# Kernel tuning notes

Hardware: AMD Instinct MI355X
Metric: run time of the kernel (lower is better)

Reference implementation:

```python
import jax, jax.numpy as jnp
import numpy as np

N_BINS = 64
SIGMA_SCALE = 0.5
_LAB_RANGES = {'L': (0.0, 100.0), 'a': (-128.0, 127.0), 'b': (-128.0, 127.0)}


def _channel_params(vmin, vmax, n_bins=N_BINS, sigma_scale=SIGMA_SCALE):
    delta = (vmax - vmin) / n_bins
    centers = jnp.linspace(vmin + delta / 2, vmax - delta / 2, n_bins, dtype=jnp.float32)
    sigma = jnp.float32(delta * sigma_scale)
    return centers, sigma


def rgb_to_lab(rgb):
    # rgb: (B, 3, H, W) in [0, 1] sRGB
    thr = 0.04045
    lin = jnp.where(rgb > thr, jnp.power((rgb + 0.055) / 1.055, 2.4), rgb / 12.92)
    r, g, b = lin[:, 0], lin[:, 1], lin[:, 2]
    # sRGB -> XYZ (D65)
    x = 0.412453 * r + 0.357580 * g + 0.180423 * b
    y = 0.212671 * r + 0.715160 * g + 0.072169 * b
    z = 0.019334 * r + 0.119193 * g + 0.950227 * b
    xn, zn = 0.950456, 1.088754  # D65 white (Y normalized to 1)
    x = x / xn
    z = z / zn
    eps = 0.008856
    def f(t):
        return jnp.where(t > eps, jnp.cbrt(t), 7.787 * t + 16.0 / 116.0)
    fx, fy, fz = f(x), f(y), f(z)
    L = 116.0 * fy - 16.0
    a = 500.0 * (fx - fy)
    bb = 200.0 * (fy - fz)
    return jnp.stack([L, a, bb], axis=1)  # (B, 3, H, W)


def setup_inputs() -> dict:
    key = jax.random.key(0)
    img = jax.random.uniform(key, (16, 3, 512, 512), dtype=jnp.float32)
    return {"img": img}


def reference(img) -> jnp.ndarray:
    B = img.shape[0]
    img_lab = rgb_to_lab(img)  # (B, 3, H, W)
    parts = []
    for c_idx, name in enumerate(['L', 'a', 'b']):
        centers, sigma = _channel_params(*_LAB_RANGES[name])
        pixels = img_lab[:, c_idx].reshape(B, -1)  # (B, HW)
        diff = pixels[:, :, None] - centers[None, None, :]  # (B, HW, n_bins)
        weights = jnp.exp(-(diff ** 2) / (2.0 * sigma ** 2))
        hist_unnorm = weights.sum(axis=1)  # (B, n_bins)
        hist = hist_unnorm / (hist_unnorm.sum(axis=-1, keepdims=True) + 1e-8)
        parts.append(hist)
    return jnp.concatenate(parts, axis=1)  # (B, 192)
```

## Files before the change

kernel.cpp:

```cpp
#include <hip/hip_runtime.h>
#include <cmath>

#define HW (512*512)
#define NSUB 2048
#define THREADS1 1024
#define BLKS_PER_IMG 32

__global__ __launch_bounds__(THREADS1) void count_kernel(const float* __restrict__ img,
                                                         unsigned* __restrict__ part) {
    __shared__ unsigned sh[2][3 * NSUB];
    const int tid = threadIdx.x;
    unsigned* flat = &sh[0][0];
    for (int i = tid; i < 2 * 3 * NSUB; i += THREADS1) flat[i] = 0u;
    __syncthreads();

    unsigned* h = sh[(tid >> 6) & 1];

    const int b  = blockIdx.y;
    const int bx = blockIdx.x;
    const float* base = img + (size_t)b * 3u * HW;

    const int stride = BLKS_PER_IMG * THREADS1 * 4;
    for (int p = (bx * THREADS1 + tid) * 4; p < HW; p += stride) {
        float4 r4 = *reinterpret_cast<const float4*>(base + p);
        float4 g4 = *reinterpret_cast<const float4*>(base + p + HW);
        float4 b4 = *reinterpret_cast<const float4*>(base + p + 2 * HW);
        float rr[4] = {r4.x, r4.y, r4.z, r4.w};
        float gg[4] = {g4.x, g4.y, g4.z, g4.w};
        float bl[4] = {b4.x, b4.y, b4.z, b4.w};

        #pragma unroll
        for (int k = 0; k < 4; ++k) {
            float lr = (rr[k] > 0.04045f) ? exp2f(2.4f * log2f((rr[k] + 0.055f) * (1.0f / 1.055f))) : rr[k] * (1.0f / 12.92f);
            float lg = (gg[k] > 0.04045f) ? exp2f(2.4f * log2f((gg[k] + 0.055f) * (1.0f / 1.055f))) : gg[k] * (1.0f / 12.92f);
            float lb = (bl[k] > 0.04045f) ? exp2f(2.4f * log2f((bl[k] + 0.055f) * (1.0f / 1.055f))) : bl[k] * (1.0f / 12.92f);

            float x = 0.4339530f * lr + 0.3762197f * lg + 0.1898288f * lb;
            float y = 0.2126710f * lr + 0.7151600f * lg + 0.0721690f * lb;
            float z = 0.0177578f * lr + 0.1094766f * lg + 0.8727661f * lb;

            float fx = (x > 0.008856f) ? exp2f(log2f(x) * (1.0f/3.0f)) : 7.787f * x + 16.0f/116.0f;
            float fy = (y > 0.008856f) ? exp2f(log2f(y) * (1.0f/3.0f)) : 7.787f * y + 16.0f/116.0f;
            float fz = (z > 0.008856f) ? exp2f(log2f(z) * (1.0f/3.0f)) : 7.787f * z + 16.0f/116.0f;

            int iL = (int)(2375.68f    * fy - 327.68f);
            int iA = (int)(4015.6863f  * (fx - fy) + 1028.01569f);
            int iB = (int)(1606.27451f * (fy - fz) + 1028.01569f);

            atomicAdd(&h[iL], 1u);
            atomicAdd(&h[NSUB + iA], 1u);
            atomicAdd(&h[2 * NSUB + iB], 1u);
        }
    }
    __syncthreads();

    unsigned* dst = part + ((size_t)(b * BLKS_PER_IMG + bx)) * 3 * NSUB;
    for (int i = tid; i < 3 * NSUB; i += THREADS1) dst[i] = sh[0][i] + sh[1][i];
}

__global__ __launch_bounds__(256) void conv_norm_kernel(const unsigned* __restrict__ part,
                                                        float* __restrict__ out) {
    __shared__ float sub[NSUB];
    __shared__ float hb[64];
    const int img = blockIdx.x / 3;
    const int ch  = blockIdx.x % 3;
    const int t   = threadIdx.x;

    const unsigned* p0 = part + (size_t)img * BLKS_PER_IMG * 3 * NSUB + (size_t)ch * NSUB;
    float acc8[8] = {0,0,0,0,0,0,0,0};
    for (int k = 0; k < BLKS_PER_IMG; ++k) {
        const unsigned* pk = p0 + (size_t)k * 3 * NSUB + t * 8;
        uint4 a = *reinterpret_cast<const uint4*>(pk);
        uint4 c = *reinterpret_cast<const uint4*>(pk + 4);
        acc8[0] += (float)a.x; acc8[1] += (float)a.y;
        acc8[2] += (float)a.z; acc8[3] += (float)a.w;
        acc8[4] += (float)c.x; acc8[5] += (float)c.y;
        acc8[6] += (float)c.z; acc8[7] += (float)c.w;
    }
    #pragma unroll
    for (int i = 0; i < 8; ++i) sub[t * 8 + i] = acc8[i];
    __syncthreads();

    const int j = t >> 2;
    const int q = t & 3;
    const float C = 2.8853901f;
    const float jf = (float)j + 0.5f - (0.5f / 32.0f);
    const int s_lo = 32 * j - 86;
    float acc = 0.0f;
    for (int i = 0; i < 51; ++i) {
        int ii = i + j; if (ii >= 51) ii -= 51;
        int s  = s_lo + q + 4 * ii;
        if ((unsigned)s < (unsigned)NSUB) {
            float d = (float)s * (1.0f / 32.0f) - jf;
            acc += sub[s] * exp2f(-C * d * d);
        }
    }
    acc += __shfl_xor(acc, 1, 64);
    acc += __shfl_xor(acc, 2, 64);
    if (q == 0) hb[j] = acc;
    __syncthreads();

    if (t < 64) {
        float v = hb[t];
        float s = v;
        #pragma unroll
        for (int off = 32; off >= 1; off >>= 1) s += __shfl_down(s, off, 64);
        s = __shfl(s, 0, 64);
        out[img * 192 + ch * 64 + t] = v / (s + 1e-8f);
    }
}

extern "C" void kernel_launch(void* const* d_in, const int* in_sizes, int n_in,
                              void* d_out, int out_size, void* d_ws, size_t ws_size,
                              hipStream_t stream) {
    const float* img = (const float*)d_in[0];
    float* out     = (float*)d_out;
    unsigned* part = (unsigned*)d_ws;

    const int B = in_sizes[0] / (3 * HW);

    count_kernel<<<dim3(BLKS_PER_IMG, B), THREADS1, 0, stream>>>(img, part);
    conv_norm_kernel<<<B * 3, 256, 0, stream>>>(part, out);
}
```

Before: 96.97 us.

## Move L-channel histogram atomics from shared memory to replicated global copies

```diff
diff --git a/kernel.cpp b/kernel.cpp
--- a/kernel.cpp
+++ b/kernel.cpp
@@ -5,19 +5,24 @@
 #define NSUB 2048
 #define THREADS1 1024
 #define BLKS_PER_IMG 32
+#define NLCOPY 8
 
 __global__ __launch_bounds__(THREADS1) void count_kernel(const float* __restrict__ img,
+                                                         unsigned* __restrict__ glL,
                                                          unsigned* __restrict__ part) {
-    __shared__ unsigned sh[2][3 * NSUB];
+    __shared__ unsigned sh[2][2 * NSUB];
     const int tid = threadIdx.x;
     unsigned* flat = &sh[0][0];
-    for (int i = tid; i < 2 * 3 * NSUB; i += THREADS1) flat[i] = 0u;
+    for (int i = tid; i < 4 * NSUB; i += THREADS1) flat[i] = 0u;
     __syncthreads();
 
     unsigned* h = sh[(tid >> 6) & 1];
 
     const int b  = blockIdx.y;
     const int bx = blockIdx.x;
+    const int blin = bx + b * BLKS_PER_IMG;
+    unsigned* gL = glL + ((size_t)b * NLCOPY + (blin & (NLCOPY - 1))) * NSUB;
+
     const float* base = img + (size_t)b * 3u * HW;
 
     const int stride = BLKS_PER_IMG * THREADS1 * 4;
@@ -47,18 +52,19 @@
             int iA = (int)(4015.6863f  * (fx - fy) + 1028.01569f);
             int iB = (int)(1606.27451f * (fy - fz) + 1028.01569f);
 
-            atomicAdd(&h[iL], 1u);
-            atomicAdd(&h[NSUB + iA], 1u);
-            atomicAdd(&h[2 * NSUB + iB], 1u);
+            atomicAdd(gL + iL, 1u);
+            atomicAdd(&h[iA], 1u);
+            atomicAdd(&h[NSUB + iB], 1u);
         }
     }
     __syncthreads();
 
-    unsigned* dst = part + ((size_t)(b * BLKS_PER_IMG + bx)) * 3 * NSUB;
-    for (int i = tid; i < 3 * NSUB; i += THREADS1) dst[i] = sh[0][i] + sh[1][i];
+    unsigned* dst = part + (size_t)blin * 2 * NSUB;
+    for (int i = tid; i < 2 * NSUB; i += THREADS1) dst[i] = sh[0][i] + sh[1][i];
 }
 
-__global__ __launch_bounds__(256) void conv_norm_kernel(const unsigned* __restrict__ part,
+__global__ __launch_bounds__(256) void conv_norm_kernel(const unsigned* __restrict__ glL,
+                                                        const unsigned* __restrict__ part,
                                                         float* __restrict__ out) {
     __shared__ float sub[NSUB];
     __shared__ float hb[64];
@@ -66,16 +72,29 @@
     const int ch  = blockIdx.x % 3;
     const int t   = threadIdx.x;
 
-    const unsigned* p0 = part + (size_t)img * BLKS_PER_IMG * 3 * NSUB + (size_t)ch * NSUB;
     float acc8[8] = {0,0,0,0,0,0,0,0};
-    for (int k = 0; k < BLKS_PER_IMG; ++k) {
-        const unsigned* pk = p0 + (size_t)k * 3 * NSUB + t * 8;
-        uint4 a = *reinterpret_cast<const uint4*>(pk);
-        uint4 c = *reinterpret_cast<const uint4*>(pk + 4);
-        acc8[0] += (float)a.x; acc8[1] += (float)a.y;
-        acc8[2] += (float)a.z; acc8[3] += (float)a.w;
-        acc8[4] += (float)c.x; acc8[5] += (float)c.y;
-        acc8[6] += (float)c.z; acc8[7] += (float)c.w;
+    if (ch == 0) {
+        const unsigned* g0 = glL + (size_t)img * NLCOPY * NSUB;
+        for (int c = 0; c < NLCOPY; ++c) {
+            const unsigned* pc = g0 + (size_t)c * NSUB + t * 8;
+            uint4 a = *reinterpret_cast<const uint4*>(pc);
+            uint4 d = *reinterpret_cast<const uint4*>(pc + 4);
+            acc8[0] += (float)a.x; acc8[1] += (float)a.y;
+            acc8[2] += (float)a.z; acc8[3] += (float)a.w;
+            acc8[4] += (float)d.x; acc8[5] += (float)d.y;
+            acc8[6] += (float)d.z; acc8[7] += (float)d.w;
+        }
+    } else {
+        const unsigned* p0 = part + (size_t)img * BLKS_PER_IMG * 2 * NSUB + (size_t)(ch - 1) * NSUB;
+        for (int k = 0; k < BLKS_PER_IMG; ++k) {
+            const unsigned* pk = p0 + (size_t)k * 2 * NSUB + t * 8;
+            uint4 a = *reinterpret_cast<const uint4*>(pk);
+            uint4 d = *reinterpret_cast<const uint4*>(pk + 4);
+            acc8[0] += (float)a.x; acc8[1] += (float)a.y;
+            acc8[2] += (float)a.z; acc8[3] += (float)a.w;
+            acc8[4] += (float)d.x; acc8[5] += (float)d.y;
+            acc8[6] += (float)d.z; acc8[7] += (float)d.w;
+        }
     }
     #pragma unroll
     for (int i = 0; i < 8; ++i) sub[t * 8 + i] = acc8[i];
@@ -115,10 +134,12 @@
                               hipStream_t stream) {
     const float* img = (const float*)d_in[0];
     float* out     = (float*)d_out;
-    unsigned* part = (unsigned*)d_ws;
+    unsigned* glL  = (unsigned*)d_ws;
+    unsigned* part = glL + (size_t)16 * NLCOPY * NSUB;
 
     const int B = in_sizes[0] / (3 * HW);
 
-    count_kernel<<<dim3(BLKS_PER_IMG, B), THREADS1, 0, stream>>>(img, part);
-    conv_norm_kernel<<<B * 3, 256, 0, stream>>>(part, out);
+    (void)hipMemsetAsync(glL, 0, (size_t)B * NLCOPY * NSUB * sizeof(unsigned), stream);
+    count_kernel<<<dim3(BLKS_PER_IMG, B), THREADS1, 0, stream>>>(img, glL, part);
+    conv_norm_kernel<<<B * 3, 256, 0, stream>>>(glL, part, out);
 }
```

After: 243.2 us. +150.8%, slower.
